# Kernel tuning notes

Hardware: AMD Instinct MI355X
Metric: run time of the kernel (lower is better)

The kernel has to match this reference:

```python
import jax, jax.numpy as jnp
import numpy as np

NUM_GROUPS = 32
EPS = 1e-6

def group_norm(x, gamma, beta):
    b, c, h, w = x.shape
    xg = x.reshape(b, NUM_GROUPS, c // NUM_GROUPS, h, w)
    mean = xg.mean(axis=(2, 3, 4), keepdims=True)
    var = xg.var(axis=(2, 3, 4), keepdims=True)
    xg = (xg - mean) * jax.lax.rsqrt(var + EPS)
    x = xg.reshape(b, c, h, w)
    return x * gamma[None, :, None, None] + beta[None, :, None, None]

def conv1x1(x, w, b):
    # x: [B,C,H,W], w: [Cout,Cin], b: [Cout]
    return jnp.einsum('bchw,oc->bohw', x, w) + b[None, :, None, None]

def setup_inputs() -> dict:
    key = jax.random.key(0)
    ks = jax.random.split(key, 11)
    B, C, H, W = 4, 512, 64, 64
    s = 1.0 / np.sqrt(C)
    return {
        'x': jax.random.normal(ks[0], (B, C, H, W), dtype=jnp.float32),
        'gn_gamma': jnp.ones((C,), jnp.float32),
        'gn_beta': jnp.zeros((C,), jnp.float32),
        'wq': jax.random.normal(ks[1], (C, C), jnp.float32) * s,
        'bq': jnp.zeros((C,), jnp.float32),
        'wk': jax.random.normal(ks[2], (C, C), jnp.float32) * s,
        'bk': jnp.zeros((C,), jnp.float32),
        'wv': jax.random.normal(ks[3], (C, C), jnp.float32) * s,
        'bv': jnp.zeros((C,), jnp.float32),
        'wo': jax.random.normal(ks[4], (C, C), jnp.float32) * s,
        'bo': jnp.zeros((C,), jnp.float32),
    }

def reference(x, gn_gamma, gn_beta, wq, bq, wk, bk, wv, bv, wo, bo):
    b, c, H, W = x.shape
    h = group_norm(x, gn_gamma, gn_beta)
    q = conv1x1(h, wq, bq).reshape(b, c, H * W).transpose(0, 2, 1)  # [B, HW, C]
    k = conv1x1(h, wk, bk).reshape(b, c, H * W)                      # [B, C, HW]
    v = conv1x1(h, wv, bv).reshape(b, c, H * W).transpose(0, 2, 1)  # [B, HW, C]
    attn = jnp.einsum('bnc,bcm->bnm', q, k) * (c ** -0.5)            # [B, HW, HW]
    attn = jax.nn.softmax(attn, axis=-1)
    out = jnp.einsum('bnm,bmc->bnc', attn, v)                        # [B, HW, C]
    out = out.transpose(0, 2, 1).reshape(b, c, H, W)
    return x + conv1x1(out, wo, bo)
```

## Files before the change

kernel.cpp:

```cpp
#include <hip/hip_runtime.h>
#include <cstdint>
#include <cstddef>

typedef __attribute__((ext_vector_type(8))) short short8;
typedef __attribute__((ext_vector_type(4))) float f32x4;
typedef __attribute__((ext_vector_type(16))) float f32x16;

#define C_ 512
#define S_ 4096
#define B_ 4
#define EPS_ 1e-6f
#define SCALE_ 0.04419417382415922f

__device__ __forceinline__ ushort f2bf(float f) {
    union { float f; uint32_t u; } v; v.f = f;
    uint32_t r = v.u + 0x7FFFu + ((v.u >> 16) & 1u);
    return (ushort)(r >> 16);
}

__global__ void wconv_kernel(const float* __restrict__ wq, const float* __restrict__ wk,
                             const float* __restrict__ wv, const float* __restrict__ wo,
                             ushort* __restrict__ out) {
    int i = blockIdx.x * 256 + threadIdx.x;
    out[i]          = f2bf(wq[i]);
    out[262144 + i] = f2bf(wk[i]);
    out[524288 + i] = f2bf(wv[i]);
    out[786432 + i] = f2bf(wo[i]);
}

__global__ __launch_bounds__(512) void gn_stats_kernel(const float* __restrict__ x,
                                                       float* __restrict__ stats) {
    int bg = blockIdx.x;
    const float* xp = x + (size_t)bg * 16 * S_;
    float sum = 0.f, ss = 0.f;
    for (int i = threadIdx.x; i < 16 * S_; i += 512) {
        float v = xp[i];
        sum += v; ss += v * v;
    }
    #pragma unroll
    for (int off = 32; off; off >>= 1) {
        sum += __shfl_down(sum, off);
        ss  += __shfl_down(ss, off);
    }
    __shared__ float r0[8], r1[8];
    int wid = threadIdx.x >> 6;
    if ((threadIdx.x & 63) == 0) { r0[wid] = sum; r1[wid] = ss; }
    __syncthreads();
    if (threadIdx.x == 0) {
        float ts = 0.f, tq = 0.f;
        #pragma unroll
        for (int w = 0; w < 8; w++) { ts += r0[w]; tq += r1[w]; }
        float mean = ts / 65536.f;
        float var  = tq / 65536.f - mean * mean;
        stats[bg * 2]     = mean;
        stats[bg * 2 + 1] = rsqrtf(var + EPS_);
    }
}

__global__ __launch_bounds__(256) void gn_apply_kernel(const float* __restrict__ x,
        const float* __restrict__ gamma, const float* __restrict__ beta,
        const float* __restrict__ stats, ushort* __restrict__ h_t) {
    int sc = blockIdx.x, g = blockIdx.y, b = blockIdx.z;
    int c0 = g * 16;
    int bg = b * 32 + g;
    float mean = stats[bg * 2], rstd = stats[bg * 2 + 1];
    int t = threadIdx.x;
    __shared__ float tile[16][257];
    const float* xp = x + ((size_t)b * C_ + c0) * S_ + sc * 256;
    {
        int c = t >> 4, s0 = (t & 15) * 4;
        const float* src = xp + (size_t)c * S_;
        #pragma unroll
        for (int j = 0; j < 4; j++) {
            float4 d = *(const float4*)(src + s0 + 64 * j);
            tile[c][s0 + 64 * j + 0] = d.x;
            tile[c][s0 + 64 * j + 1] = d.y;
            tile[c][s0 + 64 * j + 2] = d.z;
            tile[c][s0 + 64 * j + 3] = d.w;
        }
    }
    __syncthreads();
    {
        float vv[16];
        #pragma unroll
        for (int ci = 0; ci < 16; ci++) {
            float a = rstd * gamma[c0 + ci];
            float bb2 = beta[c0 + ci] - mean * a;
            vv[ci] = tile[ci][t] * a + bb2;
        }
        uint4 lo, hi;
        lo.x = (uint32_t)f2bf(vv[0])  | ((uint32_t)f2bf(vv[1])  << 16);
        lo.y = (uint32_t)f2bf(vv[2])  | ((uint32_t)f2bf(vv[3])  << 16);
        lo.z = (uint32_t)f2bf(vv[4])  | ((uint32_t)f2bf(vv[5])  << 16);
        lo.w = (uint32_t)f2bf(vv[6])  | ((uint32_t)f2bf(vv[7])  << 16);
        hi.x = (uint32_t)f2bf(vv[8])  | ((uint32_t)f2bf(vv[9])  << 16);
        hi.y = (uint32_t)f2bf(vv[10]) | ((uint32_t)f2bf(vv[11]) << 16);
        hi.z = (uint32_t)f2bf(vv[12]) | ((uint32_t)f2bf(vv[13]) << 16);
        hi.w = (uint32_t)f2bf(vv[14]) | ((uint32_t)f2bf(vv[15]) << 16);
        ushort* dst = h_t + ((size_t)b * S_ + sc * 256 + t) * C_ + c0;
        *(uint4*)dst = lo;
        *(uint4*)(dst + 8) = hi;
    }
}

template <int MODE>
__global__ __launch_bounds__(256, 2) void gemm_kernel(
        const ushort* __restrict__ A,
        const ushort* __restrict__ Bt,
        const float* __restrict__ bias,
        void* __restrict__ outp,
        const float* __restrict__ xres,
        float scale) {
    int bb = blockIdx.z;
    int m0 = blockIdx.y * 64;
    int n0 = blockIdx.x * 128;
    const ushort* Bp = Bt + (size_t)bb * S_ * C_ + (size_t)n0 * C_;
    __shared__ ushort Al[64 * 64];
    __shared__ ushort Bl[128 * 64];
    int t = threadIdx.x, lane = t & 63, wid = t >> 6;
    int wm = (wid >> 1) * 32, wn = (wid & 1) * 64;
    f32x4 acc[2][4] = {};
    for (int k0 = 0; k0 < 512; k0 += 64) {
        #pragma unroll
        for (int i = 0; i < 2; i++) {
            int cid = t + i * 256;
            int row = cid >> 3, cc = cid & 7;
            uint4 d = *(const uint4*)(A + (size_t)(m0 + row) * 512 + k0 + cc * 8);
            *(uint4*)((char*)Al + row * 128 + ((cc * 16) ^ ((row & 7) << 4))) = d;
        }
        #pragma unroll
        for (int i = 0; i < 4; i++) {
            int cid = t + i * 256;
            int row = cid >> 3, cc = cid & 7;
            uint4 d = *(const uint4*)(Bp + (size_t)row * 512 + k0 + cc * 8);
            *(uint4*)((char*)Bl + row * 128 + ((cc * 16) ^ ((row & 7) << 4))) = d;
        }
        __syncthreads();
        #pragma unroll
        for (int ks = 0; ks < 2; ks++) {
            short8 af[2], bfrag[4];
            #pragma unroll
            for (int i = 0; i < 2; i++) {
                int row = wm + i * 16 + (lane & 15);
                af[i] = *(const short8*)((char*)Al + row * 128 + ((ks * 64 + (lane >> 4) * 16) ^ ((row & 7) << 4)));
            }
            #pragma unroll
            for (int j = 0; j < 4; j++) {
                int row = wn + j * 16 + (lane & 15);
                bfrag[j] = *(const short8*)((char*)Bl + row * 128 + ((ks * 64 + (lane >> 4) * 16) ^ ((row & 7) << 4)));
            }
            #pragma unroll
            for (int i = 0; i < 2; i++)
                #pragma unroll
                for (int j = 0; j < 4; j++)
                    acc[i][j] = __builtin_amdgcn_mfma_f32_16x16x32_bf16(af[i], bfrag[j], acc[i][j], 0, 0, 0);
        }
        __syncthreads();
    }
    int rr = (lane >> 4) * 4;
    #pragma unroll
    for (int i = 0; i < 2; i++) {
        int mb = m0 + wm + i * 16 + rr;
        float bs[4];
        #pragma unroll
        for (int r = 0; r < 4; r++) bs[r] = bias[mb + r];
        #pragma unroll
        for (int j = 0; j < 4; j++) {
            int n = n0 + wn + j * 16 + (lane & 15);
            if (MODE == 0) {
                ushort* O = (ushort*)outp + (size_t)bb * S_ * C_ + (size_t)n * C_ + mb;
                uint2 pp;
                pp.x = (uint32_t)f2bf((acc[i][j][0] + bs[0]) * scale) |
                       ((uint32_t)f2bf((acc[i][j][1] + bs[1]) * scale) << 16);
                pp.y = (uint32_t)f2bf((acc[i][j][2] + bs[2]) * scale) |
                       ((uint32_t)f2bf((acc[i][j][3] + bs[3]) * scale) << 16);
                *(uint2*)O = pp;
            } else if (MODE == 1) {
                ushort* O = (ushort*)outp + (size_t)bb * C_ * S_ + (size_t)mb * S_ + n;
                #pragma unroll
                for (int r = 0; r < 4; r++) O[(size_t)r * S_] = f2bf(acc[i][j][r] + bs[r]);
            } else {
                float* O = (float*)outp + (size_t)bb * C_ * S_ + (size_t)mb * S_ + n;
                const float* X = xres + (size_t)bb * C_ * S_ + (size_t)mb * S_ + n;
                #pragma unroll
                for (int r = 0; r < 4; r++) O[(size_t)r * S_] = X[(size_t)r * S_] + acc[i][j][r] + bs[r];
            }
        }
    }
}

#define KLDS_SZ  65536
#define SLDS_OFF 65536
#define PLDS_OFF 100352
#define STM_OFF  109568

__device__ __forceinline__ void stage_k(const ushort* kp, int kv0, int wid, int lane, char* K_lds) {
    #pragma unroll
    for (int p = 0; p < 8; p++) {
        int row = wid * 8 + p;
        const char* src = (const char*)(kp + (size_t)(kv0 + row) * C_) + ((lane * 16) ^ ((row & 7) << 4));
        __builtin_amdgcn_global_load_lds(
            (const __attribute__((address_space(1))) unsigned int*)src,
            (__attribute__((address_space(3))) unsigned int*)(K_lds + row * 1024),
            16, 0, 0);
    }
}

__global__ __launch_bounds__(512, 2) void attn_kernel(const ushort* __restrict__ q_t,
        const ushort* __restrict__ k_t, const ushort* __restrict__ v,
        ushort* __restrict__ ao_t) {
    constexpr int NIT = S_ / 64;
    int qb = blockIdx.x, bb = blockIdx.y;
    int s0 = qb * 64;
    const ushort* qp = q_t + (size_t)bb * S_ * C_;
    const ushort* kp = k_t + (size_t)bb * S_ * C_;
    const ushort* vp = v   + (size_t)bb * C_ * S_;

    extern __shared__ char lds[];
    char*  K_lds = lds;
    float* S_lds = (float*)(lds + SLDS_OFF);
    char*  P_lds = lds + PLDS_OFF;
    float* st_m  = (float*)(lds + STM_OFF);
    float* st_l  = st_m + 64;
    float* st_f  = st_m + 128;

    int t = threadIdx.x, lane = t & 63, wid = t >> 6;
    int l31 = lane & 31, lh = lane >> 5;
    int qt = (wid >> 2) & 1, nt = (wid >> 1) & 1, ch = wid & 1;

    if (t < 64) { st_m[t] = -1e30f; st_l[t] = 0.f; }

    short8 qf[16];
    {
        const ushort* qrow = qp + (size_t)(s0 + qt * 32 + l31) * C_ + ch * 256 + lh * 8;
        #pragma unroll
        for (int ks = 0; ks < 16; ks++)
            qf[ks] = *(const short8*)(qrow + ks * 16);
    }
    f32x16 o_[2][2] = {};

    stage_k(kp, 0, wid, lane, K_lds);
    __syncthreads();

    for (int it = 0; it < NIT; it++) {
        int kv0 = it * 64;
        f32x16 sacc = {};
        {
            int krow = nt * 32 + l31;
            const char* kb = K_lds + krow * 1024;
            int sw = (krow & 7) << 4;
            int cb0 = ch * 512 + lh * 16;
            #pragma unroll
            for (int ks = 0; ks < 16; ks++) {
                short8 kf = *(const short8*)(kb + ((cb0 + ks * 32) ^ sw));
                sacc = __builtin_amdgcn_mfma_f32_32x32x16_bf16(qf[ks], kf, sacc, 0, 0, 0);
            }
        }
        {
            float* Sp = S_lds + (size_t)(ch * 64 + qt * 32) * 68 + nt * 32 + l31;
            #pragma unroll
            for (int r = 0; r < 16; r++) {
                int qrow = (r & 3) + 8 * (r >> 2) + 4 * lh;
                Sp[qrow * 68] = sacc[r];
            }
        }
        __syncthreads();

        if (it + 1 < NIT)
            stage_k(kp, kv0 + 64, wid, lane, K_lds);

        {
            int row = t >> 3, j = t & 7;
            const float* s0p = S_lds + (size_t)row * 68 + j * 8;
            const float* s1p = s0p + 64 * 68;
            float sv[8];
            #pragma unroll
            for (int i = 0; i < 8; i++) sv[i] = s0p[i] + s1p[i];
            float mx = sv[0];
            #pragma unroll
            for (int i = 1; i < 8; i++) mx = fmaxf(mx, sv[i]);
            mx = fmaxf(mx, __shfl_xor(mx, 1));
            mx = fmaxf(mx, __shfl_xor(mx, 2));
            mx = fmaxf(mx, __shfl_xor(mx, 4));
            float mold = st_m[row];
            float mnew = fmaxf(mold, mx);
            float ps = 0.f;
            uint32_t pk[4];
            #pragma unroll
            for (int i = 0; i < 4; i++) {
                float p0 = __expf(sv[2 * i]     - mnew);
                float p1 = __expf(sv[2 * i + 1] - mnew);
                ps += p0 + p1;
                pk[i] = (uint32_t)f2bf(p0) | ((uint32_t)f2bf(p1) << 16);
            }
            *(uint4*)(P_lds + (size_t)row * 144 + j * 16) = *(uint4*)pk;
            ps += __shfl_xor(ps, 1); ps += __shfl_xor(ps, 2); ps += __shfl_xor(ps, 4);
            float f = __expf(mold - mnew);
            if (j == 0) {
                st_m[row] = mnew;
                st_l[row] = st_l[row] * f + ps;
                st_f[row] = f;
            }
        }
        __syncthreads();

        {
            #pragma unroll
            for (int qt2 = 0; qt2 < 2; qt2++) {
                float fr[16];
                #pragma unroll
                for (int r = 0; r < 16; r++)
                    fr[r] = st_f[qt2 * 32 + (r & 3) + 8 * (r >> 2) + 4 * lh];
                #pragma unroll
                for (int dt = 0; dt < 2; dt++)
                    #pragma unroll
                    for (int r = 0; r < 16; r++)
                        o_[qt2][dt][r] *= fr[r];
            }
            short8 vb[2][4];
            const ushort* vdb = vp + (size_t)(wid * 64 + l31) * S_ + kv0 + lh * 8;
            #pragma unroll
            for (int dt = 0; dt < 2; dt++)
                #pragma unroll
                for (int ks2 = 0; ks2 < 4; ks2++)
                    vb[dt][ks2] = *(const short8*)(vdb + (size_t)dt * 32 * S_ + ks2 * 16);
            short8 pa[2][4];
            #pragma unroll
            for (int qt2 = 0; qt2 < 2; qt2++)
                #pragma unroll
                for (int ks2 = 0; ks2 < 4; ks2++)
                    pa[qt2][ks2] = *(const short8*)(P_lds + (size_t)(qt2 * 32 + l31) * 144 + ks2 * 32 + lh * 16);
            #pragma unroll
            for (int qt2 = 0; qt2 < 2; qt2++)
                #pragma unroll
                for (int dt = 0; dt < 2; dt++)
                    #pragma unroll
                    for (int ks2 = 0; ks2 < 4; ks2++)
                        o_[qt2][dt] = __builtin_amdgcn_mfma_f32_32x32x16_bf16(pa[qt2][ks2], vb[dt][ks2], o_[qt2][dt], 0, 0, 0);
        }
        __syncthreads();
    }

    #pragma unroll
    for (int qt2 = 0; qt2 < 2; qt2++) {
        float rl[16];
        #pragma unroll
        for (int r = 0; r < 16; r++)
            rl[r] = 1.0f / st_l[qt2 * 32 + (r & 3) + 8 * (r >> 2) + 4 * lh];
        #pragma unroll
        for (int dt = 0; dt < 2; dt++) {
            int d = wid * 64 + dt * 32 + l31;
            #pragma unroll
            for (int r = 0; r < 16; r++) {
                int q = qt2 * 32 + (r & 3) + 8 * (r >> 2) + 4 * lh;
                ao_t[((size_t)bb * S_ + s0 + q) * C_ + d] = f2bf(o_[qt2][dt][r] * rl[r]);
            }
        }
    }
}

extern "C" void kernel_launch(void* const* d_in, const int* in_sizes, int n_in,
                              void* d_out, int out_size, void* d_ws, size_t ws_size,
                              hipStream_t stream) {
    const float* x  = (const float*)d_in[0];
    const float* gg = (const float*)d_in[1];
    const float* gb = (const float*)d_in[2];
    const float* wq = (const float*)d_in[3];
    const float* bq = (const float*)d_in[4];
    const float* wk = (const float*)d_in[5];
    const float* bk = (const float*)d_in[6];
    const float* wv = (const float*)d_in[7];
    const float* bv = (const float*)d_in[8];
    const float* wo = (const float*)d_in[9];
    const float* bo = (const float*)d_in[10];
    float* out = (float*)d_out;

    char* ws = (char*)d_ws;
    const size_t BUF = (size_t)B_ * S_ * C_ * 2;
    ushort* h_t  = (ushort*)(ws);
    ushort* q_t  = (ushort*)(ws + BUF);
    ushort* k_t  = (ushort*)(ws + 2 * BUF);
    ushort* v_n  = (ushort*)(ws + 3 * BUF);
    ushort* ao_t = (ushort*)(ws + 4 * BUF);
    ushort* wb   = (ushort*)(ws + 5 * BUF);
    float* stats = (float*)(ws + 5 * BUF + 4 * 524288);

    wconv_kernel<<<1024, 256, 0, stream>>>(wq, wk, wv, wo, wb);
    gn_stats_kernel<<<128, 512, 0, stream>>>(x, stats);
    gn_apply_kernel<<<dim3(16, 32, B_), 256, 0, stream>>>(x, gg, gb, stats, h_t);

    dim3 ggrid(32, 8, B_);
    gemm_kernel<0><<<ggrid, 256, 0, stream>>>(wb,          h_t, bq, (void*)q_t, nullptr, SCALE_);
    gemm_kernel<0><<<ggrid, 256, 0, stream>>>(wb + 262144, h_t, bk, (void*)k_t, nullptr, 1.0f);
    gemm_kernel<1><<<ggrid, 256, 0, stream>>>(wb + 524288, h_t, bv, (void*)v_n, nullptr, 1.0f);

    attn_kernel<<<dim3(64, B_), 512, 110336, stream>>>(q_t, k_t, v_n, ao_t);

    gemm_kernel<2><<<ggrid, 256, 0, stream>>>(wb + 786432, ao_t, bo, (void*)out, x, 1.0f);
}
```

Baseline: 497.0 us.

## Double-buffer K tiles in attention, prefetch V early, store scores as fp16

New measurement: 467.4 us. 1.06x faster.

```diff
diff --git a/kernel.cpp b/kernel.cpp
--- a/kernel.cpp
+++ b/kernel.cpp
@@ -3,6 +3,7 @@
 #include <cstddef>
 
 typedef __attribute__((ext_vector_type(8))) short short8;
+typedef __attribute__((ext_vector_type(8))) _Float16 half8;
 typedef __attribute__((ext_vector_type(4))) float f32x4;
 typedef __attribute__((ext_vector_type(16))) float f32x16;
 
@@ -189,19 +190,19 @@
     }
 }
 
-#define KLDS_SZ  65536
-#define SLDS_OFF 65536
-#define PLDS_OFF 100352
-#define STM_OFF  109568
-
-__device__ __forceinline__ void stage_k(const ushort* kp, int kv0, int wid, int lane, char* K_lds) {
+#define KBUF_SZ  65536
+#define SLDS_OFF 131072
+#define PLDS_OFF 149504
+#define STM_OFF  158720
+
+__device__ __forceinline__ void stage_k(const ushort* kp, int kv0, int wid, int lane, char* Kbuf) {
     #pragma unroll
     for (int p = 0; p < 8; p++) {
         int row = wid * 8 + p;
         const char* src = (const char*)(kp + (size_t)(kv0 + row) * C_) + ((lane * 16) ^ ((row & 7) << 4));
         __builtin_amdgcn_global_load_lds(
             (const __attribute__((address_space(1))) unsigned int*)src,
-            (__attribute__((address_space(3))) unsigned int*)(K_lds + row * 1024),
+            (__attribute__((address_space(3))) unsigned int*)(Kbuf + row * 1024),
             16, 0, 0);
     }
 }
@@ -217,8 +218,9 @@
     const ushort* vp = v   + (size_t)bb * C_ * S_;
 
     extern __shared__ char lds[];
-    char*  K_lds = lds;
-    float* S_lds = (float*)(lds + SLDS_OFF);
+    char* Kbuf0 = lds;
+    char* Kbuf1 = lds + KBUF_SZ;
+    _Float16* S_lds = (_Float16*)(lds + SLDS_OFF);
     char*  P_lds = lds + PLDS_OFF;
     float* st_m  = (float*)(lds + STM_OFF);
     float* st_l  = st_m + 64;
@@ -239,15 +241,32 @@
     }
     f32x16 o_[2][2] = {};
 
-    stage_k(kp, 0, wid, lane, K_lds);
-    __syncthreads();
+    stage_k(kp, 0, wid, lane, Kbuf0);
+    asm volatile("s_waitcnt vmcnt(0) lgkmcnt(0)" ::: "memory");
+    __builtin_amdgcn_s_barrier();
+    asm volatile("" ::: "memory");
 
     for (int it = 0; it < NIT; it++) {
         int kv0 = it * 64;
+        char* Kcur = (it & 1) ? Kbuf1 : Kbuf0;
+        char* Knxt = (it & 1) ? Kbuf0 : Kbuf1;
+
+        short8 vb[2][4];
+        {
+            const ushort* vdb = vp + (size_t)(wid * 64 + l31) * S_ + kv0 + lh * 8;
+            #pragma unroll
+            for (int dt = 0; dt < 2; dt++)
+                #pragma unroll
+                for (int ks2 = 0; ks2 < 4; ks2++)
+                    vb[dt][ks2] = *(const short8*)(vdb + (size_t)dt * 32 * S_ + ks2 * 16);
+        }
+        if (it + 1 < NIT)
+            stage_k(kp, kv0 + 64, wid, lane, Knxt);
+
         f32x16 sacc = {};
         {
             int krow = nt * 32 + l31;
-            const char* kb = K_lds + krow * 1024;
+            const char* kb = Kcur + krow * 1024;
             int sw = (krow & 7) << 4;
             int cb0 = ch * 512 + lh * 16;
             #pragma unroll
@@ -257,25 +276,24 @@
             }
         }
         {
-            float* Sp = S_lds + (size_t)(ch * 64 + qt * 32) * 68 + nt * 32 + l31;
+            _Float16* Sp = S_lds + (size_t)ch * 4608 + (size_t)(qt * 32) * 72 + nt * 32 + l31;
             #pragma unroll
             for (int r = 0; r < 16; r++) {
                 int qrow = (r & 3) + 8 * (r >> 2) + 4 * lh;
-                Sp[qrow * 68] = sacc[r];
-            }
-        }
-        __syncthreads();
-
-        if (it + 1 < NIT)
-            stage_k(kp, kv0 + 64, wid, lane, K_lds);
+                Sp[qrow * 72] = (_Float16)sacc[r];
+            }
+        }
+        asm volatile("s_waitcnt lgkmcnt(0)" ::: "memory");
+        __builtin_amdgcn_s_barrier();
+        asm volatile("" ::: "memory");
 
         {
             int row = t >> 3, j = t & 7;
-            const float* s0p = S_lds + (size_t)row * 68 + j * 8;
-            const float* s1p = s0p + 64 * 68;
+            half8 h0 = *(const half8*)((const char*)S_lds + (size_t)row * 144 + j * 16);
+            half8 h1 = *(const half8*)((const char*)S_lds + 9216 + (size_t)row * 144 + j * 16);
             float sv[8];
             #pragma unroll
-            for (int i = 0; i < 8; i++) sv[i] = s0p[i] + s1p[i];
+            for (int i = 0; i < 8; i++) sv[i] = (float)h0[i] + (float)h1[i];
             float mx = sv[0];
             #pragma unroll
             for (int i = 1; i < 8; i++) mx = fmaxf(mx, sv[i]);
@@ -302,28 +320,28 @@
                 st_f[row] = f;
             }
         }
-        __syncthreads();
+        asm volatile("s_waitcnt lgkmcnt(0)" ::: "memory");
+        __builtin_amdgcn_s_barrier();
+        asm volatile("" ::: "memory");
 
         {
             #pragma unroll
             for (int qt2 = 0; qt2 < 2; qt2++) {
+                f32x4 f0 = *(const f32x4*)(st_f + qt2 * 32 + 0  + 4 * lh);
+                f32x4 f1 = *(const f32x4*)(st_f + qt2 * 32 + 8  + 4 * lh);
+                f32x4 f2 = *(const f32x4*)(st_f + qt2 * 32 + 16 + 4 * lh);
+                f32x4 f3 = *(const f32x4*)(st_f + qt2 * 32 + 24 + 4 * lh);
                 float fr[16];
                 #pragma unroll
-                for (int r = 0; r < 16; r++)
-                    fr[r] = st_f[qt2 * 32 + (r & 3) + 8 * (r >> 2) + 4 * lh];
+                for (int e = 0; e < 4; e++) {
+                    fr[e] = f0[e]; fr[4 + e] = f1[e]; fr[8 + e] = f2[e]; fr[12 + e] = f3[e];
+                }
                 #pragma unroll
                 for (int dt = 0; dt < 2; dt++)
                     #pragma unroll
                     for (int r = 0; r < 16; r++)
                         o_[qt2][dt][r] *= fr[r];
             }
-            short8 vb[2][4];
-            const ushort* vdb = vp + (size_t)(wid * 64 + l31) * S_ + kv0 + lh * 8;
-            #pragma unroll
-            for (int dt = 0; dt < 2; dt++)
-                #pragma unroll
-                for (int ks2 = 0; ks2 < 4; ks2++)
-                    vb[dt][ks2] = *(const short8*)(vdb + (size_t)dt * 32 * S_ + ks2 * 16);
             short8 pa[2][4];
             #pragma unroll
             for (int qt2 = 0; qt2 < 2; qt2++)
@@ -338,15 +356,23 @@
                     for (int ks2 = 0; ks2 < 4; ks2++)
                         o_[qt2][dt] = __builtin_amdgcn_mfma_f32_32x32x16_bf16(pa[qt2][ks2], vb[dt][ks2], o_[qt2][dt], 0, 0, 0);
         }
-        __syncthreads();
+        asm volatile("s_waitcnt vmcnt(0) lgkmcnt(0)" ::: "memory");
+        __builtin_amdgcn_s_barrier();
+        asm volatile("" ::: "memory");
     }
 
     #pragma unroll
     for (int qt2 = 0; qt2 < 2; qt2++) {
+        f32x4 l0 = *(const f32x4*)(st_l + qt2 * 32 + 0  + 4 * lh);
+        f32x4 l1 = *(const f32x4*)(st_l + qt2 * 32 + 8  + 4 * lh);
+        f32x4 l2 = *(const f32x4*)(st_l + qt2 * 32 + 16 + 4 * lh);
+        f32x4 l3 = *(const f32x4*)(st_l + qt2 * 32 + 24 + 4 * lh);
         float rl[16];
         #pragma unroll
-        for (int r = 0; r < 16; r++)
-            rl[r] = 1.0f / st_l[qt2 * 32 + (r & 3) + 8 * (r >> 2) + 4 * lh];
+        for (int e = 0; e < 4; e++) {
+            rl[e] = 1.0f / l0[e]; rl[4 + e] = 1.0f / l1[e];
+            rl[8 + e] = 1.0f / l2[e]; rl[12 + e] = 1.0f / l3[e];
+        }
         #pragma unroll
         for (int dt = 0; dt < 2; dt++) {
             int d = wid * 64 + dt * 32 + l31;
@@ -394,7 +420,7 @@
     gemm_kernel<0><<<ggrid, 256, 0, stream>>>(wb + 262144, h_t, bk, (void*)k_t, nullptr, 1.0f);
     gemm_kernel<1><<<ggrid, 256, 0, stream>>>(wb + 524288, h_t, bv, (void*)v_n, nullptr, 1.0f);
 
-    attn_kernel<<<dim3(64, B_), 512, 110336, stream>>>(q_t, k_t, v_n, ao_t);
+    attn_kernel<<<dim3(64, B_), 512, 159488, stream>>>(q_t, k_t, v_n, ao_t);
 
     gemm_kernel<2><<<ggrid, 256, 0, stream>>>(wb + 786432, ao_t, bo, (void*)out, x, 1.0f);
 }
```
